# Optimization experiments

Hardware: AMD Instinct MI355X
Metric: run time of the kernel (lower is better)

## Reference

```python
import jax, jax.numpy as jnp
import numpy as np

OUT_FEATURES = 4096
IN_FEATURES = 4096
NNZ = 1677722
BATCH, SEQ = 2, 2048


def setup_inputs() -> dict:
    key = jax.random.key(0)
    k1, k2, k3, k4 = jax.random.split(key, 4)
    x = jax.random.normal(k1, (BATCH, SEQ, IN_FEATURES), dtype=jnp.float32)
    data = jax.random.normal(k2, (NNZ,), dtype=jnp.float32)
    rows = jax.random.randint(k3, (NNZ,), 0, OUT_FEATURES, dtype=jnp.int32)
    cols = jax.random.randint(k4, (NNZ,), 0, IN_FEATURES, dtype=jnp.int32)
    return {"x": x, "data": data, "rows": rows, "cols": cols}


def reference(x, data, rows, cols):
    # Densify sparse weight W [out_features, in_features] from COO triples
    # (equivalent math to the CSR spmm in the original module).
    W = jnp.zeros((OUT_FEATURES, IN_FEATURES), dtype=data.dtype)
    W = W.at[rows, cols].add(data)
    # Original: (W @ x_flat.T).T reshaped -> y = x @ W^T, shape [B, S, out]
    return jnp.einsum("bsi,oi->bso", x, W)
```

## Files before the change

### kernel.cpp

```cpp
#include <hip/hip_runtime.h>
#include <stdint.h>

#define M_ROWS 4096
#define N_OUT  4096
#define K_IN   4096
#define NNZ_N  1677722
#define NBLK_A 128
#define CHUNK_A 13108
#define NBINS  512

typedef __attribute__((ext_vector_type(8))) short  bf16x8_t;
typedef __attribute__((ext_vector_type(4))) float  f32x4_t;

__device__ __forceinline__ unsigned short f2bf(float f) {
    union { float f; uint32_t u; } v; v.f = f;
    uint32_t u = v.u;
    u += 0x7FFFu + ((u >> 16) & 1u);
    return (unsigned short)(u >> 16);
}

__global__ void convert_x(const float4* __restrict__ x, uint4* __restrict__ xo) {
    int i = blockIdx.x * blockDim.x + threadIdx.x;
    float4 a = x[2 * i], b = x[2 * i + 1];
    uint4 o;
    o.x = (uint32_t)f2bf(a.x) | ((uint32_t)f2bf(a.y) << 16);
    o.y = (uint32_t)f2bf(a.z) | ((uint32_t)f2bf(a.w) << 16);
    o.z = (uint32_t)f2bf(b.x) | ((uint32_t)f2bf(b.y) << 16);
    o.w = (uint32_t)f2bf(b.z) | ((uint32_t)f2bf(b.w) << 16);
    xo[i] = o;
}

__global__ __launch_bounds__(1024) void sort_local(const float* __restrict__ data,
                                                   const int* __restrict__ rows,
                                                   const int* __restrict__ cols,
                                                   uint32_t* __restrict__ run,
                                                   uint32_t* __restrict__ Fbase) {
    __shared__ uint32_t hist[NBINS];
    __shared__ uint32_t basev[NBINS];
    __shared__ uint32_t cur[NBINS];
    __shared__ uint32_t ebuf[CHUNK_A];
    const int blk   = blockIdx.x, t = threadIdx.x;
    const int start = blk * CHUNK_A;
    const int end   = min(start + CHUNK_A, NNZ_N);
    const int nloc  = end - start;

    for (int j = t; j < NBINS; j += 1024) hist[j] = 0;
    __syncthreads();
    for (int i = start + t; i < end; i += 1024)
        atomicAdd(&hist[rows[i] >> 3], 1u);
    __syncthreads();

    if (t < 64) {
        uint32_t pre[8], loc = 0;
#pragma unroll
        for (int q = 0; q < 8; ++q) { pre[q] = loc; loc += hist[t * 8 + q]; }
        uint32_t x = loc;
#pragma unroll
        for (int off = 1; off < 64; off <<= 1) {
            uint32_t y = __shfl_up(x, off);
            if (t >= off) x += y;
        }
        uint32_t excl = x - loc;
#pragma unroll
        for (int q = 0; q < 8; ++q) {
            basev[t * 8 + q] = excl + pre[q];
            cur[t * 8 + q]   = excl + pre[q];
        }
    }
    __syncthreads();

    for (int i = start + t; i < end; i += 1024) {
        int r = rows[i];
        uint32_t slot = atomicAdd(&cur[r >> 3], 1u);
        ebuf[slot] = ((uint32_t)(r & 7) << 28) |
                     ((uint32_t)cols[i] << 16) | (uint32_t)f2bf(data[i]);
    }
    __syncthreads();

    for (int j = t; j < nloc; j += 1024)
        run[start + j] = ebuf[j];
    if (t < NBINS) Fbase[(size_t)t * NBLK_A + blk] = basev[t];
    if (t == 0)    Fbase[(size_t)NBINS * NBLK_A + blk] = (uint32_t)nloc;
}

__global__ __launch_bounds__(512) void accum_bins(const uint32_t* __restrict__ run,
                                                  const uint32_t* __restrict__ Fbase,
                                                  unsigned short* __restrict__ W) {
    __shared__ float    acc[8 * K_IN];
    __shared__ uint32_t segS[NBLK_A], segE[NBLK_A];
    const int f = blockIdx.x, t = threadIdx.x;

    float4* av = (float4*)acc;
    for (int j = t; j < 8 * K_IN / 4; j += 512) av[j] = (float4){0.f, 0.f, 0.f, 0.f};
    if (t < NBLK_A)                    segS[t]          = Fbase[(size_t)f * NBLK_A + t];
    else if (t < 2 * NBLK_A)           segE[t - NBLK_A] = Fbase[(size_t)(f + 1) * NBLK_A + (t - NBLK_A)];
    __syncthreads();

    const int wave = t >> 6, lane = t & 63;
    for (int blk = wave; blk < NBLK_A; blk += 8) {
        uint32_t s = segS[blk], e = segE[blk];
        const uint32_t* rp = run + (size_t)blk * CHUNK_A;
        for (uint32_t j = s + lane; j < e; j += 64) {
            uint32_t en = rp[j];
            union { uint32_t u; float fv; } v; v.u = (en & 0xFFFFu) << 16;
            atomicAdd(&acc[((en >> 28) & 7u) * K_IN + ((en >> 16) & 0xFFFu)], v.fv);
        }
    }
    __syncthreads();

    uint4* wv = (uint4*)(W + (size_t)f * 8 * K_IN);
    for (int j = t; j < 8 * K_IN / 8; j += 512) {
        float4 a = av[2 * j], c = av[2 * j + 1];
        uint4 o;
        o.x = (uint32_t)f2bf(a.x) | ((uint32_t)f2bf(a.y) << 16);
        o.y = (uint32_t)f2bf(a.z) | ((uint32_t)f2bf(a.w) << 16);
        o.z = (uint32_t)f2bf(c.x) | ((uint32_t)f2bf(c.y) << 16);
        o.w = (uint32_t)f2bf(c.z) | ((uint32_t)f2bf(c.w) << 16);
        wv[j] = o;
    }
}

__device__ __forceinline__ void async_ld16(const void* g, void* lds_wave_base) {
    __builtin_amdgcn_global_load_lds(
        (const __attribute__((address_space(1))) uint32_t*)g,
        (__attribute__((address_space(3))) uint32_t*)lds_wave_base,
        16, 0, 0);
}

#define STAGE_M(gbase, lbase, kt, slot) do {                                   \
    const unsigned short* g_ = (gbase) + (kt) * 64;                            \
    unsigned short*       l_ = (lbase) + (slot) * 32768;                       \
    async_ld16(g_,                  l_);                                       \
    async_ld16(g_ + 1 * 64 * K_IN,  l_ + 4096);                                \
    async_ld16(g_ + 2 * 64 * K_IN,  l_ + 8192);                                \
    async_ld16(g_ + 3 * 64 * K_IN,  l_ + 12288);                               \
} while (0)

__global__ __launch_bounds__(512, 2) void gemm_bt(const unsigned short* __restrict__ A,
                                                  const unsigned short* __restrict__ B,
                                                  float* __restrict__ C) {
    __shared__ __align__(16) unsigned short lds_[65536];

    const int t    = threadIdx.x;
    const int wave = t >> 6;
    const int lane = t & 63;
    const int wr   = wave >> 2;
    const int wc   = wave & 3;
    const int m0   = blockIdx.y * 256;
    const int n0   = blockIdx.x * 256;

    const int srow = t >> 3;
    const int sch  = ((t & 7) ^ (srow & 7)) * 8;
    const unsigned short* gA = A + (size_t)(m0 + srow) * K_IN + sch;
    const unsigned short* gB = B + (size_t)(n0 + srow) * K_IN + sch;
    unsigned short* lA = lds_ + wave * 512;
    unsigned short* lB = lds_ + 16384 + wave * 512;

    const int l15  = lane & 15;
    const int aoff = (wr * 128 + l15) * 64;
    const int boff = (wc * 64  + l15) * 64;
    const int ck0  = (((lane >> 4)    ) ^ (lane & 7)) * 8;
    const int ck1  = (((lane >> 4) | 4) ^ (lane & 7)) * 8;

    f32x4_t acc[8][4];
#pragma unroll
    for (int i = 0; i < 8; ++i)
#pragma unroll
        for (int j = 0; j < 4; ++j) acc[i][j] = (f32x4_t){0.f, 0.f, 0.f, 0.f};

    bf16x8_t af[4][2], bf0[2][2], bf1[2][2];

    STAGE_M(gA, lA, 0, 0); STAGE_M(gB, lB, 0, 0);
    STAGE_M(gA, lA, 1, 1); STAGE_M(gB, lB, 1, 1);
    asm volatile("s_waitcnt vmcnt(8)" ::: "memory");
    __builtin_amdgcn_s_barrier();

    for (int kt = 0; kt < 64; ++kt) {
        const unsigned short* pA = lds_ + (kt & 1) * 32768;
        const unsigned short* pB = pA + 16384;

#pragma unroll
        for (int im = 0; im < 4; ++im) {
            af[im][0] = *(const bf16x8_t*)(pA + aoff + im * 1024 + ck0);
            af[im][1] = *(const bf16x8_t*)(pA + aoff + im * 1024 + ck1);
        }
#pragma unroll
        for (int jn = 0; jn < 2; ++jn) {
            bf0[jn][0] = *(const bf16x8_t*)(pB + boff + jn * 1024 + ck0);
            bf0[jn][1] = *(const bf16x8_t*)(pB + boff + jn * 1024 + ck1);
        }
        __builtin_amdgcn_s_barrier();
        asm volatile("s_waitcnt lgkmcnt(0)" ::: "memory");
        __builtin_amdgcn_s_setprio(1);
#pragma unroll
        for (int im = 0; im < 4; ++im)
#pragma unroll
            for (int jn = 0; jn < 2; ++jn)
#pragma unroll
                for (int kk = 0; kk < 2; ++kk)
                    acc[im][jn] = __builtin_amdgcn_mfma_f32_16x16x32_bf16(
                        af[im][kk], bf0[jn][kk], acc[im][jn], 0, 0, 0);
        __builtin_amdgcn_s_setprio(0);
        __builtin_amdgcn_s_barrier();

#pragma unroll
        for (int jn = 0; jn < 2; ++jn) {
            bf1[jn][0] = *(const bf16x8_t*)(pB + boff + (2 + jn) * 1024 + ck0);
            bf1[jn][1] = *(const bf16x8_t*)(pB + boff + (2 + jn) * 1024 + ck1);
        }
        __builtin_amdgcn_s_barrier();
        asm volatile("s_waitcnt lgkmcnt(0)" ::: "memory");
        __builtin_amdgcn_s_setprio(1);
#pragma unroll
        for (int im = 0; im < 4; ++im)
#pragma unroll
            for (int jn = 0; jn < 2; ++jn)
#pragma unroll
                for (int kk = 0; kk < 2; ++kk)
                    acc[im][2 + jn] = __builtin_amdgcn_mfma_f32_16x16x32_bf16(
                        af[im][kk], bf1[jn][kk], acc[im][2 + jn], 0, 0, 0);
        __builtin_amdgcn_s_setprio(0);
        __builtin_amdgcn_s_barrier();

        if (kt < 62) STAGE_M(gB, lB, kt + 2, (kt & 1));
#pragma unroll
        for (int im = 0; im < 4; ++im) {
            af[im][0] = *(const bf16x8_t*)(pA + aoff + (4 + im) * 1024 + ck0);
            af[im][1] = *(const bf16x8_t*)(pA + aoff + (4 + im) * 1024 + ck1);
        }
        __builtin_amdgcn_s_barrier();
        asm volatile("s_waitcnt lgkmcnt(0)" ::: "memory");
        __builtin_amdgcn_s_setprio(1);
#pragma unroll
        for (int im = 0; im < 4; ++im)
#pragma unroll
            for (int jn = 0; jn < 2; ++jn)
#pragma unroll
                for (int kk = 0; kk < 2; ++kk)
                    acc[4 + im][jn] = __builtin_amdgcn_mfma_f32_16x16x32_bf16(
                        af[im][kk], bf0[jn][kk], acc[4 + im][jn], 0, 0, 0);
        __builtin_amdgcn_s_setprio(0);
        __builtin_amdgcn_s_barrier();

        if (kt < 62) STAGE_M(gA, lA, kt + 2, (kt & 1));
        __builtin_amdgcn_s_setprio(1);
#pragma unroll
        for (int im = 0; im < 4; ++im)
#pragma unroll
            for (int jn = 0; jn < 2; ++jn)
#pragma unroll
                for (int kk = 0; kk < 2; ++kk)
                    acc[4 + im][2 + jn] = __builtin_amdgcn_mfma_f32_16x16x32_bf16(
                        af[im][kk], bf1[jn][kk], acc[4 + im][2 + jn], 0, 0, 0);
        __builtin_amdgcn_s_setprio(0);
        if (kt < 62) {
            asm volatile("s_waitcnt vmcnt(8)" ::: "memory");
        } else {
            asm volatile("s_waitcnt vmcnt(0)" ::: "memory");
        }
        __builtin_amdgcn_s_barrier();
    }

    const int crow = m0 + wr * 128 + ((lane >> 4) << 2);
    const int ccol = n0 + wc * 64 + l15;
#pragma unroll
    for (int im = 0; im < 8; ++im)
#pragma unroll
        for (int jn = 0; jn < 4; ++jn)
#pragma unroll
            for (int r = 0; r < 4; ++r)
                C[(size_t)(crow + im * 16 + r) * N_OUT + ccol + jn * 16] =
                    acc[im][jn][r];
}

extern "C" void kernel_launch(void* const* d_in, const int* in_sizes, int n_in,
                              void* d_out, int out_size, void* d_ws, size_t ws_size,
                              hipStream_t stream) {
    const float* x    = (const float*)d_in[0];
    const float* data = (const float*)d_in[1];
    const int*   rows = (const int*)d_in[2];
    const int*   cols = (const int*)d_in[3];
    float*       out  = (float*)d_out;

    unsigned short* W_bf16 = (unsigned short*)d_ws;
    unsigned short* x_bf16 = (unsigned short*)((char*)d_ws + (32u << 20));
    uint32_t*       run    = (uint32_t*)((char*)d_ws + (64u << 20));
    uint32_t*       Fbase  = (uint32_t*)((char*)d_ws + (72u << 20));

    convert_x<<<(M_ROWS * K_IN) / (8 * 256), 256, 0, stream>>>(
        (const float4*)x, (uint4*)x_bf16);

    sort_local<<<NBLK_A, 1024, 0, stream>>>(data, rows, cols, run, Fbase);

    accum_bins<<<NBINS, 512, 0, stream>>>(run, Fbase, W_bf16);

    dim3 grid(N_OUT / 256, M_ROWS / 256);
    gemm_bt<<<grid, 512, 0, stream>>>(x_bf16, W_bf16, out);
}
```

Baseline: 288.1 us.

## Fuse x conversion, COO bin sort and W densify into one cooperative kernel

Merges the x-to-bf16 conversion, the per-chunk row-bin sort and the shared-memory W accumulation into a single cooperative kernel of 256 blocks, with a grid-wide sync between the sort and accumulation phases. This removes two launches and their gaps, and spreads the sort over 256 blocks with smaller chunks. Each block now densifies two 8-row bins in sequence, using workgroup-scoped atomics. If the cooperative launch fails, it falls back to two ordinary launches. The cost is one block per CU, a grid barrier, and the serial two-bin loop, which may cut parallelism in the accumulation phase.

```diff
diff --git a/kernel.cpp b/kernel.cpp
--- a/kernel.cpp
+++ b/kernel.cpp
@@ -1,12 +1,15 @@
 #include <hip/hip_runtime.h>
+#include <hip/hip_cooperative_groups.h>
 #include <stdint.h>
+
+namespace cg = cooperative_groups;
 
 #define M_ROWS 4096
 #define N_OUT  4096
 #define K_IN   4096
 #define NNZ_N  1677722
-#define NBLK_A 128
-#define CHUNK_A 13108
+#define NBLK   256
+#define CHUNK  6560
 #define NBINS  512
 
 typedef __attribute__((ext_vector_type(8))) short  bf16x8_t;
@@ -19,104 +22,107 @@
     return (unsigned short)(u >> 16);
 }
 
-__global__ void convert_x(const float4* __restrict__ x, uint4* __restrict__ xo) {
-    int i = blockIdx.x * blockDim.x + threadIdx.x;
-    float4 a = x[2 * i], b = x[2 * i + 1];
-    uint4 o;
-    o.x = (uint32_t)f2bf(a.x) | ((uint32_t)f2bf(a.y) << 16);
-    o.y = (uint32_t)f2bf(a.z) | ((uint32_t)f2bf(a.w) << 16);
-    o.z = (uint32_t)f2bf(b.x) | ((uint32_t)f2bf(b.y) << 16);
-    o.w = (uint32_t)f2bf(b.z) | ((uint32_t)f2bf(b.w) << 16);
-    xo[i] = o;
-}
-
-__global__ __launch_bounds__(1024) void sort_local(const float* __restrict__ data,
-                                                   const int* __restrict__ rows,
-                                                   const int* __restrict__ cols,
-                                                   uint32_t* __restrict__ run,
-                                                   uint32_t* __restrict__ Fbase) {
-    __shared__ uint32_t hist[NBINS];
-    __shared__ uint32_t basev[NBINS];
-    __shared__ uint32_t cur[NBINS];
-    __shared__ uint32_t ebuf[CHUNK_A];
-    const int blk   = blockIdx.x, t = threadIdx.x;
-    const int start = blk * CHUNK_A;
-    const int end   = min(start + CHUNK_A, NNZ_N);
-    const int nloc  = end - start;
-
-    for (int j = t; j < NBINS; j += 1024) hist[j] = 0;
-    __syncthreads();
-    for (int i = start + t; i < end; i += 1024)
-        atomicAdd(&hist[rows[i] >> 3], 1u);
-    __syncthreads();
-
-    if (t < 64) {
-        uint32_t pre[8], loc = 0;
-#pragma unroll
-        for (int q = 0; q < 8; ++q) { pre[q] = loc; loc += hist[t * 8 + q]; }
-        uint32_t x = loc;
-#pragma unroll
-        for (int off = 1; off < 64; off <<= 1) {
-            uint32_t y = __shfl_up(x, off);
-            if (t >= off) x += y;
-        }
-        uint32_t excl = x - loc;
-#pragma unroll
-        for (int q = 0; q < 8; ++q) {
-            basev[t * 8 + q] = excl + pre[q];
-            cur[t * 8 + q]   = excl + pre[q];
-        }
-    }
-    __syncthreads();
-
-    for (int i = start + t; i < end; i += 1024) {
-        int r = rows[i];
-        uint32_t slot = atomicAdd(&cur[r >> 3], 1u);
-        ebuf[slot] = ((uint32_t)(r & 7) << 28) |
-                     ((uint32_t)cols[i] << 16) | (uint32_t)f2bf(data[i]);
-    }
-    __syncthreads();
-
-    for (int j = t; j < nloc; j += 1024)
-        run[start + j] = ebuf[j];
-    if (t < NBINS) Fbase[(size_t)t * NBLK_A + blk] = basev[t];
-    if (t == 0)    Fbase[(size_t)NBINS * NBLK_A + blk] = (uint32_t)nloc;
-}
-
-__global__ __launch_bounds__(512) void accum_bins(const uint32_t* __restrict__ run,
-                                                  const uint32_t* __restrict__ Fbase,
-                                                  unsigned short* __restrict__ W) {
-    __shared__ float    acc[8 * K_IN];
-    __shared__ uint32_t segS[NBLK_A], segE[NBLK_A];
-    const int f = blockIdx.x, t = threadIdx.x;
-
-    float4* av = (float4*)acc;
-    for (int j = t; j < 8 * K_IN / 4; j += 512) av[j] = (float4){0.f, 0.f, 0.f, 0.f};
-    if (t < NBLK_A)                    segS[t]          = Fbase[(size_t)f * NBLK_A + t];
-    else if (t < 2 * NBLK_A)           segE[t - NBLK_A] = Fbase[(size_t)(f + 1) * NBLK_A + (t - NBLK_A)];
-    __syncthreads();
-
+__global__ __launch_bounds__(1024, 1) void prep_fused(
+        const float4* __restrict__ x, const float* __restrict__ data,
+        const int* __restrict__ rows, const int* __restrict__ cols,
+        uint4* __restrict__ xo, uint32_t* __restrict__ run,
+        uint32_t* __restrict__ Fbase, unsigned short* __restrict__ W, int mask) {
+    __shared__ __align__(16) float pool[8 * K_IN];
+    __shared__ uint32_t hist[NBINS], basev[NBINS], curv[NBINS];
+    const int blk = blockIdx.x, t = threadIdx.x;
     const int wave = t >> 6, lane = t & 63;
-    for (int blk = wave; blk < NBLK_A; blk += 8) {
-        uint32_t s = segS[blk], e = segE[blk];
-        const uint32_t* rp = run + (size_t)blk * CHUNK_A;
-        for (uint32_t j = s + lane; j < e; j += 64) {
-            uint32_t en = rp[j];
-            union { uint32_t u; float fv; } v; v.u = (en & 0xFFFFu) << 16;
-            atomicAdd(&acc[((en >> 28) & 7u) * K_IN + ((en >> 16) & 0xFFFu)], v.fv);
-        }
-    }
-    __syncthreads();
-
-    uint4* wv = (uint4*)(W + (size_t)f * 8 * K_IN);
-    for (int j = t; j < 8 * K_IN / 8; j += 512) {
-        float4 a = av[2 * j], c = av[2 * j + 1];
-        uint4 o;
-        o.x = (uint32_t)f2bf(a.x) | ((uint32_t)f2bf(a.y) << 16);
-        o.y = (uint32_t)f2bf(a.z) | ((uint32_t)f2bf(a.w) << 16);
-        o.z = (uint32_t)f2bf(c.x) | ((uint32_t)f2bf(c.y) << 16);
-        o.w = (uint32_t)f2bf(c.z) | ((uint32_t)f2bf(c.w) << 16);
-        wv[j] = o;
+
+    if (mask & 1) {
+        const int gsz = NBLK * 1024;
+        for (int i = blk * 1024 + t; i < M_ROWS * K_IN / 8; i += gsz) {
+            float4 a = x[2 * i], b = x[2 * i + 1];
+            uint4 o;
+            o.x = (uint32_t)f2bf(a.x) | ((uint32_t)f2bf(a.y) << 16);
+            o.y = (uint32_t)f2bf(a.z) | ((uint32_t)f2bf(a.w) << 16);
+            o.z = (uint32_t)f2bf(b.x) | ((uint32_t)f2bf(b.y) << 16);
+            o.w = (uint32_t)f2bf(b.z) | ((uint32_t)f2bf(b.w) << 16);
+            xo[i] = o;
+        }
+        uint32_t* ebuf = (uint32_t*)pool;
+        const int start = blk * CHUNK;
+        const int end   = (start + CHUNK < NNZ_N) ? start + CHUNK : NNZ_N;
+        const int nloc  = end - start;
+        for (int j = t; j < NBINS; j += 1024) hist[j] = 0;
+        __syncthreads();
+        for (int i = start + t; i < end; i += 1024)
+            atomicAdd(&hist[rows[i] >> 3], 1u);
+        __syncthreads();
+        if (t < 64) {
+            uint32_t pre[8], loc = 0;
+#pragma unroll
+            for (int q = 0; q < 8; ++q) { pre[q] = loc; loc += hist[t * 8 + q]; }
+            uint32_t xv = loc;
+#pragma unroll
+            for (int off = 1; off < 64; off <<= 1) {
+                uint32_t y = __shfl_up(xv, off);
+                if (t >= off) xv += y;
+            }
+            uint32_t excl = xv - loc;
+#pragma unroll
+            for (int q = 0; q < 8; ++q) {
+                basev[t * 8 + q] = excl + pre[q];
+                curv[t * 8 + q]  = excl + pre[q];
+            }
+        }
+        __syncthreads();
+        for (int i = start + t; i < end; i += 1024) {
+            int r = rows[i];
+            uint32_t slot = atomicAdd(&curv[r >> 3], 1u);
+            ebuf[slot] = ((uint32_t)(r & 7) << 28) |
+                         ((uint32_t)cols[i] << 16) | (uint32_t)f2bf(data[i]);
+        }
+        __syncthreads();
+        for (int j = t; j < nloc; j += 1024) run[start + j] = ebuf[j];
+        if (t < NBINS) Fbase[(size_t)t * NBLK + blk] = basev[t];
+        if (t == 0)    Fbase[(size_t)NBINS * NBLK + blk] = (uint32_t)nloc;
+    }
+
+    if (mask == 3) {
+        __threadfence();
+        cg::this_grid().sync();
+    }
+
+    if (mask & 2) {
+        uint32_t* segS = hist;
+        uint32_t* segE = basev;
+        float4*   av   = (float4*)pool;
+#pragma unroll 1
+        for (int rep = 0; rep < 2; ++rep) {
+            const int f = blk * 2 + rep;
+            for (int j = t; j < 8 * K_IN / 4; j += 1024)
+                av[j] = (float4){0.f, 0.f, 0.f, 0.f};
+            if (t < NBLK)           segS[t] = Fbase[(size_t)f * NBLK + t];
+            else if (t < 2 * NBLK)  segE[t - NBLK] = Fbase[(size_t)(f + 1) * NBLK + (t - NBLK)];
+            __syncthreads();
+            for (int b2 = wave; b2 < NBLK; b2 += 16) {
+                uint32_t s = segS[b2], e = segE[b2];
+                const uint32_t* rp = run + (size_t)b2 * CHUNK;
+                for (uint32_t j = s + lane; j < e; j += 64) {
+                    uint32_t en = rp[j];
+                    union { uint32_t u; float fv; } v; v.u = (en & 0xFFFFu) << 16;
+                    __hip_atomic_fetch_add(
+                        &pool[((en >> 28) & 7u) * K_IN + ((en >> 16) & 0xFFFu)],
+                        v.fv, __ATOMIC_RELAXED, __HIP_MEMORY_SCOPE_WORKGROUP);
+                }
+            }
+            __syncthreads();
+            uint4* wv = (uint4*)(W + (size_t)f * 8 * K_IN);
+            for (int j = t; j < 8 * K_IN / 8; j += 1024) {
+                float4 a = av[2 * j], c = av[2 * j + 1];
+                uint4 o;
+                o.x = (uint32_t)f2bf(a.x) | ((uint32_t)f2bf(a.y) << 16);
+                o.y = (uint32_t)f2bf(a.z) | ((uint32_t)f2bf(a.w) << 16);
+                o.z = (uint32_t)f2bf(c.x) | ((uint32_t)f2bf(c.y) << 16);
+                o.w = (uint32_t)f2bf(c.z) | ((uint32_t)f2bf(c.w) << 16);
+                wv[j] = o;
+            }
+            __syncthreads();
+        }
     }
 }
 
@@ -287,12 +293,21 @@
     uint32_t*       run    = (uint32_t*)((char*)d_ws + (64u << 20));
     uint32_t*       Fbase  = (uint32_t*)((char*)d_ws + (72u << 20));
 
-    convert_x<<<(M_ROWS * K_IN) / (8 * 256), 256, 0, stream>>>(
-        (const float4*)x, (uint4*)x_bf16);
-
-    sort_local<<<NBLK_A, 1024, 0, stream>>>(data, rows, cols, run, Fbase);
-
-    accum_bins<<<NBINS, 512, 0, stream>>>(run, Fbase, W_bf16);
+    const float4* x4 = (const float4*)x;
+    uint4*        xo = (uint4*)x_bf16;
+    int mask = 3;
+    void* args[] = {(void*)&x4, (void*)&data, (void*)&rows, (void*)&cols,
+                    (void*)&xo, (void*)&run, (void*)&Fbase, (void*)&W_bf16,
+                    (void*)&mask};
+    hipError_t e = hipLaunchCooperativeKernel((const void*)prep_fused,
+                                              dim3(NBLK), dim3(1024),
+                                              args, 0, stream);
+    if (e != hipSuccess) {
+        prep_fused<<<NBLK, 1024, 0, stream>>>(x4, data, rows, cols, xo,
+                                              run, Fbase, W_bf16, 1);
+        prep_fused<<<NBLK, 1024, 0, stream>>>(x4, data, rows, cols, xo,
+                                              run, Fbase, W_bf16, 2);
+    }
 
     dim3 grid(N_OUT / 256, M_ROWS / 256);
     gemm_bt<<<grid, 512, 0, stream>>>(x_bf16, W_bf16, out);
```

Measured after the change: 423.1 us. +46.8%, slower.
